# Performance work log

Hardware: AMD Instinct MI355X
Metric: run time of the kernel (lower is better)

Reference implementation:

```python
import jax, jax.numpy as jnp
import numpy as np
import math

B, N, WIDTH, HEADS = 2, 2048, 1024, 16
ATTN_CH = WIDTH // HEADS  # 64 (note: width//heads//3 of the 3*width fused dim)


def setup_inputs() -> dict:
    key = jax.random.key(0)
    ks = jax.random.split(key, 3)
    std = 0.02
    return {
        "x": jax.random.normal(ks[0], (B, N, WIDTH), dtype=jnp.float32),
        "w_qkv": jax.random.normal(ks[1], (WIDTH, 3 * WIDTH), dtype=jnp.float32) * std,
        "b_qkv": jnp.zeros((3 * WIDTH,), dtype=jnp.float32),
        "w_proj": jax.random.normal(ks[2], (WIDTH, WIDTH), dtype=jnp.float32) * std,
        "b_proj": jnp.zeros((WIDTH,), dtype=jnp.float32),
    }


def reference(x, w_qkv, b_qkv, w_proj, b_proj):
    bs, n_ctx, width = x.shape
    qkv = x @ w_qkv + b_qkv                       # [b, n, 3*width]
    attn_ch = (3 * width) // HEADS // 3           # head dim
    scale = 1.0 / math.sqrt(math.sqrt(attn_ch))
    # per-head layout: [b, n, heads, 3*attn_ch] -> split q,k,v
    qkv = qkv.reshape(bs, n_ctx, HEADS, 3 * attn_ch)
    q, k, v = jnp.split(qkv, 3, axis=-1)          # each [b, n, h, c]
    weight = jnp.einsum("bthc,bshc->bhts", q * scale, k * scale)
    weight = jax.nn.softmax(weight.astype(jnp.float32), axis=-1).astype(qkv.dtype)
    out = jnp.einsum("bhts,bshc->bthc", weight, v).reshape(bs, n_ctx, -1)
    return out @ w_proj + b_proj
```

## Files before the change

### kernel.cpp

```cpp
#include <hip/hip_runtime.h>
#include <hip/hip_fp16.h>

#define BATCH 2
#define NCTX  2048
#define WIDTH 1024
#define HEADS 16
#define CH    64
#define QKVD  (3 * WIDTH)
#define MROWS (BATCH * NCTX)

typedef __attribute__((ext_vector_type(4))) float    f32x4;
typedef __attribute__((ext_vector_type(8))) _Float16 f16x8;

#define QSCALE 0.18033688011112042f

__device__ __forceinline__ void gll16(void* lds, const void* g) {
    __builtin_amdgcn_global_load_lds(
        (const __attribute__((address_space(1))) unsigned int*)g,
        (__attribute__((address_space(3))) unsigned int*)lds, 16, 0, 0);
}

__device__ __forceinline__ unsigned pkrtz(float a, float b) {
    auto p = __builtin_amdgcn_cvt_pkrtz(a, b);
    return __builtin_bit_cast(unsigned, p);
}

__global__ __launch_bounds__(256)
void split_x_f16(const float* __restrict__ x, __half* __restrict__ tiles)
{
    const int mb = blockIdx.x, kt = blockIdx.y;
    const int t = threadIdx.x;
    __half* tb = (__half*)tiles + ((size_t)mb * 32 + kt) * 4096;
    #pragma unroll
    for (int it = 0; it < 2; ++it) {
        const int idx = it * 256 + t;
        const int m = idx >> 2, q = idx & 3;
        const float* src = x + (size_t)(mb * 128 + m) * WIDTH + kt * 32 + q * 8;
        const f32x4 v0 = *(const f32x4*)src;
        const f32x4 v1 = *(const f32x4*)(src + 4);
        f16x8 h;
        #pragma unroll
        for (int j = 0; j < 4; ++j) { h[j] = (_Float16)v0[j]; h[4 + j] = (_Float16)v1[j]; }
        *(f16x8*)&tb[(q * 128 + m) * 8] = h;
    }
}

__global__ __launch_bounds__(256)
void split_w_f16(const float* __restrict__ w, __half* __restrict__ tiles, int N)
{
    __shared__ float tile[32][129];
    const int nb = blockIdx.x, kt = blockIdx.y;
    const int t = threadIdx.x;
    #pragma unroll
    for (int it = 0; it < 2; ++it) {
        const int idx = it * 256 + t;
        const int kk = idx >> 4, n8 = idx & 15;
        const float* src = w + (size_t)(kt * 32 + kk) * N + nb * 128 + n8 * 8;
        #pragma unroll
        for (int j = 0; j < 8; ++j) tile[kk][n8 * 8 + j] = src[j];
    }
    __syncthreads();
    __half* tb = tiles + ((size_t)nb * 32 + kt) * 4096;
    #pragma unroll
    for (int it = 0; it < 2; ++it) {
        const int idx = it * 256 + t;
        const int q = idx >> 7, nn = idx & 127;
        f16x8 h;
        #pragma unroll
        for (int j = 0; j < 8; ++j) h[j] = (_Float16)tile[q * 8 + j][nn];
        *(f16x8*)&tb[(q * 128 + nn) * 8] = h;
    }
}

__global__ __launch_bounds__(256)
void gemm_qkv(const __half* __restrict__ At, const __half* __restrict__ Bt,
              const float* __restrict__ bias,
              __half* __restrict__ qg, __half* __restrict__ kg, __half* __restrict__ vtg)
{
    __shared__ __align__(16) _Float16 sm[16384];
    const int t = threadIdx.x, lane = t & 63, w = t >> 6;
    const int lq = lane & 15, quad = lane >> 4;
    const int nb = blockIdx.x, mb = blockIdx.y;
    const int wm = (w >> 1) * 64, wn = (w & 1) * 64;

    const __half* Ab = At + ((size_t)mb * 32) * 4096;
    const __half* Bb = Bt + ((size_t)nb * 32) * 4096;
    const int c0 = w * 4;

    f32x4 acc[4][4];
    #pragma unroll
    for (int i = 0; i < 4; ++i)
        #pragma unroll
        for (int j = 0; j < 4; ++j) acc[i][j] = 0;

    f16x8 pf[4];
    #pragma unroll
    for (int i = 0; i < 4; ++i) {
        const int c = c0 + i;
        const __half* g = (c < 8 ? Ab + c * 512 : Bb + (c - 8) * 512) + lane * 8;
        pf[i] = *(const f16x8*)g;
    }
    #pragma unroll
    for (int i = 0; i < 4; ++i)
        *(f16x8*)&sm[(c0 + i) * 512 + lane * 8] = pf[i];
    __syncthreads();

    for (int kt = 0; kt < 32; ++kt) {
        _Float16* cur = sm + (kt & 1) * 8192;
        _Float16* nxt = sm + ((kt + 1) & 1) * 8192;

        if (kt + 1 < 32) {
            #pragma unroll
            for (int i = 0; i < 4; ++i) {
                const int c = c0 + i;
                const __half* g = (c < 8 ? Ab + (size_t)(kt + 1) * 4096 + c * 512
                                         : Bb + (size_t)(kt + 1) * 4096 + (c - 8) * 512) + lane * 8;
                pf[i] = *(const f16x8*)g;
            }
        }

        f16x8 a[4], b[4];
        #pragma unroll
        for (int i = 0; i < 4; ++i) {
            a[i] = *(const f16x8*)&cur[(quad * 128 + wm + i * 16 + lq) * 8];
            b[i] = *(const f16x8*)&cur[4096 + (quad * 128 + wn + i * 16 + lq) * 8];
        }
        #pragma unroll
        for (int i = 0; i < 4; ++i)
            #pragma unroll
            for (int j = 0; j < 4; ++j)
                acc[i][j] = __builtin_amdgcn_mfma_f32_16x16x32_f16(a[i], b[j], acc[i][j], 0, 0, 0);

        if (kt + 1 < 32) {
            #pragma unroll
            for (int i = 0; i < 4; ++i)
                *(f16x8*)&nxt[(c0 + i) * 512 + lane * 8] = pf[i];
        }
        __syncthreads();
    }

    const int bb = mb >> 4;
    #pragma unroll
    for (int jf = 0; jf < 4; ++jf) {
        const int col = nb * 128 + wn + jf * 16 + lq;
        const int h = col / 192;
        const int sect = col - h * 192;
        const int type = sect >> 6;
        const int c = sect & 63;
        const float bv = bias[col];
        const size_t bh = (size_t)bb * 16 + h;
        #pragma unroll
        for (int i = 0; i < 4; ++i) {
            #pragma unroll
            for (int r = 0; r < 4; ++r) {
                const int n = (mb & 15) * 128 + wm + i * 16 + quad * 4 + r;
                const float v = acc[i][jf][r] + bv;
                if (type == 0) {
                    const size_t a2 = ((bh * 16 + (n >> 7)) * 8 + (c >> 3)) * 1024
                                      + (size_t)(n & 127) * 8 + (c & 7);
                    qg[a2] = __float2half(v * QSCALE);
                } else if (type == 1) {
                    const size_t a2 = ((bh * 32 + (n >> 6)) * 8 + (c >> 3)) * 512
                                      + (size_t)(n & 63) * 8 + (c & 7);
                    kg[a2] = __float2half(v);
                } else {
                    const size_t a2 = ((bh * 32 + (n >> 6)) * 8 + ((n >> 3) & 7)) * 512
                                      + (size_t)c * 8 + (n & 7);
                    vtg[a2] = __float2half(v);
                }
            }
        }
    }
}

__global__ __launch_bounds__(256)
void attn_mfma5(const __half* __restrict__ qg, const __half* __restrict__ kg,
                const __half* __restrict__ vtg, __half* __restrict__ a2)
{
    __shared__ __align__(16) _Float16 Ks[2][4096];
    __shared__ __align__(16) _Float16 Vt[2][4096];
    __shared__ __align__(16) _Float16 Ps[4096];

    const int t = threadIdx.x, lane = t & 63, w = t >> 6;
    const int lq = lane & 15, quad = lane >> 4;
    const int bid = blockIdx.x;
    const int qt = (bid >> 3) & 31;
    const int bh_ = (bid & 7) + ((bid >> 8) << 3);
    const size_t bh = (size_t)bh_;
    const int h = bh_ & 15, b = bh_ >> 4;

    const __half* qtile = qg + (bh * 16 + (qt >> 1)) * 8192 + (size_t)(qt & 1) * 512;
    const __half* kbase = kg + bh * 32 * 4096;
    const __half* vbase = vtg + bh * 32 * 4096;

    #pragma unroll
    for (int i = 0; i < 2; ++i)
        gll16((void*)&Ps[(w * 2 + i) * 512],
              (const void*)(qtile + (size_t)(w * 2 + i) * 1024 + lane * 8));

    const int lw = w * 1024 + lane * 8;
    f16x8 kpf[2], vpf[2];
    #pragma unroll
    for (int i = 0; i < 2; ++i) {
        kpf[i] = *(const f16x8*)(kbase + lw + i * 512);
        vpf[i] = *(const f16x8*)(vbase + lw + i * 512);
    }
    __syncthreads();

    #pragma unroll
    for (int i = 0; i < 2; ++i) {
        *(f16x8*)&Ks[0][lw + i * 512] = kpf[i];
        *(f16x8*)&Vt[0][lw + i * 512] = vpf[i];
    }
    f16x8 aq[2];
    #pragma unroll
    for (int ks = 0; ks < 2; ++ks)
        aq[ks] = *(const f16x8*)&Ps[((ks * 4 + quad) * 64 + w * 16 + lq) * 8];
    __syncthreads();

    f32x4 O[4], Ol;
    Ol = 0;
    #pragma unroll
    for (int j = 0; j < 4; ++j) O[j] = 0;
    f16x8 ones;
    #pragma unroll
    for (int j = 0; j < 8; ++j) ones[j] = (_Float16)1.0f;

    _Float16* Pw = &Ps[w * 1024];
    const int kb_hi = quad >> 1, joff = (quad & 1) * 4;
    const f32x4 zc = {0.0f, 0.0f, 0.0f, 0.0f};

    const __half* kp = kbase + 4096 + lw;
    const __half* vp = vbase + 4096 + lw;

    for (int kt = 0; kt < 32; ++kt) {
        const int cur = kt & 1;

        if (kt < 31) {
            kpf[0] = *(const f16x8*)(kp);
            kpf[1] = *(const f16x8*)(kp + 512);
            vpf[0] = *(const f16x8*)(vp);
            vpf[1] = *(const f16x8*)(vp + 512);
            kp += 4096; vp += 4096;
        }

        f32x4 st[4];
        #pragma unroll
        for (int mt = 0; mt < 4; ++mt) {
            f16x8 kf0 = *(const f16x8*)&Ks[cur][((quad) * 64 + mt * 16 + lq) * 8];
            f16x8 kf1 = *(const f16x8*)&Ks[cur][((4 + quad) * 64 + mt * 16 + lq) * 8];
            st[mt] = __builtin_amdgcn_mfma_f32_16x16x32_f16(kf0, aq[0], zc, 0, 0, 0);
            st[mt] = __builtin_amdgcn_mfma_f32_16x16x32_f16(kf1, aq[1], st[mt], 0, 0, 0);
        }

        #pragma unroll
        for (int mt = 0; mt < 4; ++mt) {
            const float e0 = __builtin_amdgcn_exp2f(st[mt][0]);
            const float e1 = __builtin_amdgcn_exp2f(st[mt][1]);
            const float e2 = __builtin_amdgcn_exp2f(st[mt][2]);
            const float e3 = __builtin_amdgcn_exp2f(st[mt][3]);
            uint2 pk;
            pk.x = pkrtz(e0, e1);
            pk.y = pkrtz(e2, e3);
            *(uint2*)&Pw[((mt * 2 + kb_hi) * 16 + lq) * 8 + joff] = pk;
        }

        #pragma unroll
        for (int ks = 0; ks < 2; ++ks) {
            f16x8 ap = *(const f16x8*)&Pw[((ks * 4 + quad) * 16 + lq) * 8];
            Ol = __builtin_amdgcn_mfma_f32_16x16x32_f16(ap, ones, Ol, 0, 0, 0);
            #pragma unroll
            for (int jc = 0; jc < 4; ++jc) {
                f16x8 vf = *(const f16x8*)&Vt[cur][((ks * 4 + quad) * 64 + jc * 16 + lq) * 8];
                O[jc] = __builtin_amdgcn_mfma_f32_16x16x32_f16(ap, vf, O[jc], 0, 0, 0);
            }
        }

        if (kt < 31) {
            *(f16x8*)&Ks[cur ^ 1][lw]       = kpf[0];
            *(f16x8*)&Ks[cur ^ 1][lw + 512] = kpf[1];
            *(f16x8*)&Vt[cur ^ 1][lw]       = vpf[0];
            *(f16x8*)&Vt[cur ^ 1][lw + 512] = vpf[1];
        }
        __syncthreads();
    }

    float linv[4];
    #pragma unroll
    for (int r = 0; r < 4; ++r) linv[r] = 1.0f / Ol[r];

    __half* a2t = a2 + ((size_t)(b * 16 + (qt >> 1)) * 32) * 4096;
    const int mbase = (qt & 1) * 64 + w * 16 + quad * 4;
    #pragma unroll
    for (int jc = 0; jc < 4; ++jc) {
        const int ch = h * 64 + jc * 16 + lq;
        const int ktp = ch >> 5;
        const int qc = (ch >> 3) & 3;
        const int j = ch & 7;
        #pragma unroll
        for (int r = 0; r < 4; ++r) {
            a2t[(size_t)ktp * 4096 + (qc * 128 + mbase + r) * 8 + j] =
                __float2half(O[jc][r] * linv[r]);
        }
    }
}

__global__ __launch_bounds__(256)
void gemm_proj(const __half* __restrict__ At, const __half* __restrict__ Bt,
               const float* __restrict__ bias, float* __restrict__ out)
{
    __shared__ __align__(16) _Float16 sm[16384];
    const int t = threadIdx.x, lane = t & 63, w = t >> 6;
    const int lq = lane & 15, quad = lane >> 4;
    const int nb = blockIdx.x, mb = blockIdx.y;
    const int wm = (w >> 1) * 64, wn = (w & 1) * 64;

    const __half* Ab = At + ((size_t)mb * 32) * 4096;
    const __half* Bb = Bt + ((size_t)nb * 32) * 4096;
    const int c0 = w * 4;

    f32x4 acc[4][4];
    #pragma unroll
    for (int i = 0; i < 4; ++i)
        #pragma unroll
        for (int j = 0; j < 4; ++j) acc[i][j] = 0;

    f16x8 pf[4];
    #pragma unroll
    for (int i = 0; i < 4; ++i) {
        const int c = c0 + i;
        const __half* g = (c < 8 ? Ab + c * 512 : Bb + (c - 8) * 512) + lane * 8;
        pf[i] = *(const f16x8*)g;
    }
    #pragma unroll
    for (int i = 0; i < 4; ++i)
        *(f16x8*)&sm[(c0 + i) * 512 + lane * 8] = pf[i];
    __syncthreads();

    for (int kt = 0; kt < 32; ++kt) {
        _Float16* cur = sm + (kt & 1) * 8192;
        _Float16* nxt = sm + ((kt + 1) & 1) * 8192;

        if (kt + 1 < 32) {
            #pragma unroll
            for (int i = 0; i < 4; ++i) {
                const int c = c0 + i;
                const __half* g = (c < 8 ? Ab + (size_t)(kt + 1) * 4096 + c * 512
                                         : Bb + (size_t)(kt + 1) * 4096 + (c - 8) * 512) + lane * 8;
                pf[i] = *(const f16x8*)g;
            }
        }

        f16x8 a[4], b[4];
        #pragma unroll
        for (int i = 0; i < 4; ++i) {
            a[i] = *(const f16x8*)&cur[(quad * 128 + wm + i * 16 + lq) * 8];
            b[i] = *(const f16x8*)&cur[4096 + (quad * 128 + wn + i * 16 + lq) * 8];
        }
        #pragma unroll
        for (int i = 0; i < 4; ++i)
            #pragma unroll
            for (int j = 0; j < 4; ++j)
                acc[i][j] = __builtin_amdgcn_mfma_f32_16x16x32_f16(a[i], b[j], acc[i][j], 0, 0, 0);

        if (kt + 1 < 32) {
            #pragma unroll
            for (int i = 0; i < 4; ++i)
                *(f16x8*)&nxt[(c0 + i) * 512 + lane * 8] = pf[i];
        }
        __syncthreads();
    }

    #pragma unroll
    for (int jf = 0; jf < 4; ++jf) {
        const int col = nb * 128 + wn + jf * 16 + lq;
        const float bv = bias[col];
        #pragma unroll
        for (int i = 0; i < 4; ++i)
            #pragma unroll
            for (int r = 0; r < 4; ++r) {
                const int row = mb * 128 + wm + i * 16 + quad * 4 + r;
                out[(size_t)row * WIDTH + col] = acc[i][jf][r] + bv;
            }
    }
}

extern "C" void kernel_launch(void* const* d_in, const int* in_sizes, int n_in,
                              void* d_out, int out_size, void* d_ws, size_t ws_size,
                              hipStream_t stream)
{
    const float* x      = (const float*)d_in[0];
    const float* w_qkv  = (const float*)d_in[1];
    const float* b_qkv  = (const float*)d_in[2];
    const float* w_proj = (const float*)d_in[3];
    const float* b_proj = (const float*)d_in[4];
    float* out = (float*)d_out;

    char* p = (char*)d_ws;
    size_t o = 0;
    __half* A1  = (__half*)(p + o); o += (size_t)MROWS * WIDTH * 2;
    __half* Bq  = (__half*)(p + o); o += (size_t)WIDTH * QKVD * 2;
    __half* Qg  = (__half*)(p + o); o += (size_t)MROWS * WIDTH * 2;
    __half* Kg  = (__half*)(p + o); o += (size_t)MROWS * WIDTH * 2;
    __half* Vtg = (__half*)(p + o); o += (size_t)MROWS * WIDTH * 2;
    __half* A2  = (__half*)(p + o); o += (size_t)MROWS * WIDTH * 2;
    __half* Bp  = (__half*)(p + o); o += (size_t)WIDTH * WIDTH * 2;

    dim3 blk(256);

    split_x_f16<<<dim3(32, 32), blk, 0, stream>>>(x, A1);
    split_w_f16<<<dim3(24, 32), blk, 0, stream>>>(w_qkv, Bq, QKVD);
    split_w_f16<<<dim3(8, 32),  blk, 0, stream>>>(w_proj, Bp, WIDTH);

    gemm_qkv<<<dim3(24, 32), blk, 0, stream>>>(A1, Bq, b_qkv, Qg, Kg, Vtg);

    attn_mfma5<<<dim3(1024), blk, 0, stream>>>(Qg, Kg, Vtg, A2);

    gemm_proj<<<dim3(8, 32), blk, 0, stream>>>(A2, Bp, b_proj, out);
}
```

Baseline: 205.5 us.

## Split attention KV range across waves with register-direct loads and LDS reduction

The attention kernel now gives each wave all 64 query rows of the block and a quarter of each key tile, instead of 16 query rows and the full tile. K and V fragments are loaded straight from global into registers, and the P fragment is fed to the 16x16x16 MFMA from registers, so the double-buffered LDS staging of K/V/P and the per-tile barriers go away. Partial row sums and output accumulators are then reduced across waves through LDS in two passes. This avoids the unnormalised max-free softmax rescale, but raises register pressure (64 accumulator regs plus Q fragments), uses uncoalesced 8-byte V loads, and adds an end-of-kernel reduction.

```diff
diff --git a/kernel.cpp b/kernel.cpp
--- a/kernel.cpp
+++ b/kernel.cpp
@@ -11,14 +11,9 @@
 
 typedef __attribute__((ext_vector_type(4))) float    f32x4;
 typedef __attribute__((ext_vector_type(8))) _Float16 f16x8;
+typedef __attribute__((ext_vector_type(4))) _Float16 f16x4;
 
 #define QSCALE 0.18033688011112042f
-
-__device__ __forceinline__ void gll16(void* lds, const void* g) {
-    __builtin_amdgcn_global_load_lds(
-        (const __attribute__((address_space(1))) unsigned int*)g,
-        (__attribute__((address_space(3))) unsigned int*)lds, 16, 0, 0);
-}
 
 __device__ __forceinline__ unsigned pkrtz(float a, float b) {
     auto p = __builtin_amdgcn_cvt_pkrtz(a, b);
@@ -174,12 +169,11 @@
 }
 
 __global__ __launch_bounds__(256)
-void attn_mfma5(const __half* __restrict__ qg, const __half* __restrict__ kg,
+void attn_mfma7(const __half* __restrict__ qg, const __half* __restrict__ kg,
                 const __half* __restrict__ vtg, __half* __restrict__ a2)
 {
-    __shared__ __align__(16) _Float16 Ks[2][4096];
-    __shared__ __align__(16) _Float16 Vt[2][4096];
-    __shared__ __align__(16) _Float16 Ps[4096];
+    __shared__ __align__(16) float red[4][3][2][16][16];
+    __shared__ __align__(16) float rol[4][3][16];
 
     const int t = threadIdx.x, lane = t & 63, w = t >> 6;
     const int lq = lane & 15, quad = lane >> 4;
@@ -189,119 +183,139 @@
     const size_t bh = (size_t)bh_;
     const int h = bh_ & 15, b = bh_ >> 4;
 
-    const __half* qtile = qg + (bh * 16 + (qt >> 1)) * 8192 + (size_t)(qt & 1) * 512;
+    const __half* qtile = qg + (bh * 16 + (qt >> 1)) * 8192;
     const __half* kbase = kg + bh * 32 * 4096;
     const __half* vbase = vtg + bh * 32 * 4096;
 
-    #pragma unroll
-    for (int i = 0; i < 2; ++i)
-        gll16((void*)&Ps[(w * 2 + i) * 512],
-              (const void*)(qtile + (size_t)(w * 2 + i) * 1024 + lane * 8));
-
-    const int lw = w * 1024 + lane * 8;
-    f16x8 kpf[2], vpf[2];
-    #pragma unroll
-    for (int i = 0; i < 2; ++i) {
-        kpf[i] = *(const f16x8*)(kbase + lw + i * 512);
-        vpf[i] = *(const f16x8*)(vbase + lw + i * 512);
-    }
-    __syncthreads();
-
-    #pragma unroll
-    for (int i = 0; i < 2; ++i) {
-        *(f16x8*)&Ks[0][lw + i * 512] = kpf[i];
-        *(f16x8*)&Vt[0][lw + i * 512] = vpf[i];
-    }
-    f16x8 aq[2];
-    #pragma unroll
-    for (int ks = 0; ks < 2; ++ks)
-        aq[ks] = *(const f16x8*)&Ps[((ks * 4 + quad) * 64 + w * 16 + lq) * 8];
-    __syncthreads();
-
-    f32x4 O[4], Ol;
-    Ol = 0;
-    #pragma unroll
-    for (int j = 0; j < 4; ++j) O[j] = 0;
-    f16x8 ones;
-    #pragma unroll
-    for (int j = 0; j < 8; ++j) ones[j] = (_Float16)1.0f;
-
-    _Float16* Pw = &Ps[w * 1024];
-    const int kb_hi = quad >> 1, joff = (quad & 1) * 4;
+    const int qrow0 = (qt & 1) * 64;
+    f16x8 aq[4][2];
+    #pragma unroll
+    for (int qn = 0; qn < 4; ++qn)
+        #pragma unroll
+        for (int ks = 0; ks < 2; ++ks)
+            aq[qn][ks] = *(const f16x8*)(qtile + (size_t)(ks * 4 + quad) * 1024
+                                         + (qrow0 + qn * 16 + lq) * 8);
+
+    const int kofs0 = ((0 * 4 + quad) * 64 + w * 16 + lq) * 8;
+    const int kofs1 = ((1 * 4 + quad) * 64 + w * 16 + lq) * 8;
+    int vofs[4];
+    #pragma unroll
+    for (int jc = 0; jc < 4; ++jc)
+        vofs[jc] = ((w * 2 + (quad >> 1)) * 64 + jc * 16 + lq) * 8 + (quad & 1) * 4;
+
+    f32x4 O[4][4], Ol[4];
+    #pragma unroll
+    for (int qn = 0; qn < 4; ++qn) {
+        Ol[qn] = 0;
+        #pragma unroll
+        for (int jc = 0; jc < 4; ++jc) O[qn][jc] = 0;
+    }
+    f16x4 ones4;
+    #pragma unroll
+    for (int j = 0; j < 4; ++j) ones4[j] = (_Float16)1.0f;
     const f32x4 zc = {0.0f, 0.0f, 0.0f, 0.0f};
 
-    const __half* kp = kbase + 4096 + lw;
-    const __half* vp = vbase + 4096 + lw;
+    f16x8 kf0 = *(const f16x8*)(kbase + kofs0);
+    f16x8 kf1 = *(const f16x8*)(kbase + kofs1);
+    f16x4 vf[4];
+    #pragma unroll
+    for (int jc = 0; jc < 4; ++jc) vf[jc] = *(const f16x4*)(vbase + vofs[jc]);
+
+    const __half* kp = kbase + 4096;
+    const __half* vp = vbase + 4096;
 
     for (int kt = 0; kt < 32; ++kt) {
-        const int cur = kt & 1;
-
+        f16x8 kn0, kn1; f16x4 vn[4];
         if (kt < 31) {
-            kpf[0] = *(const f16x8*)(kp);
-            kpf[1] = *(const f16x8*)(kp + 512);
-            vpf[0] = *(const f16x8*)(vp);
-            vpf[1] = *(const f16x8*)(vp + 512);
+            kn0 = *(const f16x8*)(kp + kofs0);
+            kn1 = *(const f16x8*)(kp + kofs1);
+            #pragma unroll
+            for (int jc = 0; jc < 4; ++jc) vn[jc] = *(const f16x4*)(vp + vofs[jc]);
             kp += 4096; vp += 4096;
         }
 
-        f32x4 st[4];
-        #pragma unroll
-        for (int mt = 0; mt < 4; ++mt) {
-            f16x8 kf0 = *(const f16x8*)&Ks[cur][((quad) * 64 + mt * 16 + lq) * 8];
-            f16x8 kf1 = *(const f16x8*)&Ks[cur][((4 + quad) * 64 + mt * 16 + lq) * 8];
-            st[mt] = __builtin_amdgcn_mfma_f32_16x16x32_f16(kf0, aq[0], zc, 0, 0, 0);
-            st[mt] = __builtin_amdgcn_mfma_f32_16x16x32_f16(kf1, aq[1], st[mt], 0, 0, 0);
-        }
-
-        #pragma unroll
-        for (int mt = 0; mt < 4; ++mt) {
-            const float e0 = __builtin_amdgcn_exp2f(st[mt][0]);
-            const float e1 = __builtin_amdgcn_exp2f(st[mt][1]);
-            const float e2 = __builtin_amdgcn_exp2f(st[mt][2]);
-            const float e3 = __builtin_amdgcn_exp2f(st[mt][3]);
+        #pragma unroll
+        for (int qn = 0; qn < 4; ++qn) {
+            f32x4 st = __builtin_amdgcn_mfma_f32_16x16x32_f16(kf0, aq[qn][0], zc, 0, 0, 0);
+            st = __builtin_amdgcn_mfma_f32_16x16x32_f16(kf1, aq[qn][1], st, 0, 0, 0);
+            const float e0 = __builtin_amdgcn_exp2f(st[0]);
+            const float e1 = __builtin_amdgcn_exp2f(st[1]);
+            const float e2 = __builtin_amdgcn_exp2f(st[2]);
+            const float e3 = __builtin_amdgcn_exp2f(st[3]);
             uint2 pk;
             pk.x = pkrtz(e0, e1);
             pk.y = pkrtz(e2, e3);
-            *(uint2*)&Pw[((mt * 2 + kb_hi) * 16 + lq) * 8 + joff] = pk;
-        }
-
-        #pragma unroll
-        for (int ks = 0; ks < 2; ++ks) {
-            f16x8 ap = *(const f16x8*)&Pw[((ks * 4 + quad) * 16 + lq) * 8];
-            Ol = __builtin_amdgcn_mfma_f32_16x16x32_f16(ap, ones, Ol, 0, 0, 0);
-            #pragma unroll
-            for (int jc = 0; jc < 4; ++jc) {
-                f16x8 vf = *(const f16x8*)&Vt[cur][((ks * 4 + quad) * 64 + jc * 16 + lq) * 8];
-                O[jc] = __builtin_amdgcn_mfma_f32_16x16x32_f16(ap, vf, O[jc], 0, 0, 0);
-            }
+            const f16x4 pa = __builtin_bit_cast(f16x4, pk);
+            Ol[qn] = __builtin_amdgcn_mfma_f32_16x16x16f16(pa, ones4, Ol[qn], 0, 0, 0);
+            #pragma unroll
+            for (int jc = 0; jc < 4; ++jc)
+                O[qn][jc] = __builtin_amdgcn_mfma_f32_16x16x16f16(pa, vf[jc], O[qn][jc], 0, 0, 0);
         }
 
         if (kt < 31) {
-            *(f16x8*)&Ks[cur ^ 1][lw]       = kpf[0];
-            *(f16x8*)&Ks[cur ^ 1][lw + 512] = kpf[1];
-            *(f16x8*)&Vt[cur ^ 1][lw]       = vpf[0];
-            *(f16x8*)&Vt[cur ^ 1][lw + 512] = vpf[1];
-        }
-        __syncthreads();
-    }
-
+            kf0 = kn0; kf1 = kn1;
+            #pragma unroll
+            for (int jc = 0; jc < 4; ++jc) vf[jc] = vn[jc];
+        }
+    }
+
+    #pragma unroll
+    for (int qn = 0; qn < 4; ++qn) {
+        if (qn == w) continue;
+        const int rel = (w < qn) ? w : w - 1;
+        if (lq == 0)
+            *(f32x4*)&rol[qn][rel][quad * 4] = Ol[qn];
+        *(f32x4*)&red[qn][rel][0][lq][quad * 4] = O[qn][0];
+        *(f32x4*)&red[qn][rel][1][lq][quad * 4] = O[qn][1];
+    }
+    __syncthreads();
+
+    f32x4 lt = Ol[w];
+    #pragma unroll
+    for (int s = 0; s < 3; ++s) lt += *(const f32x4*)&rol[w][s][quad * 4];
     float linv[4];
     #pragma unroll
-    for (int r = 0; r < 4; ++r) linv[r] = 1.0f / Ol[r];
+    for (int r = 0; r < 4; ++r) linv[r] = 1.0f / lt[r];
 
     __half* a2t = a2 + ((size_t)(b * 16 + (qt >> 1)) * 32) * 4096;
-    const int mbase = (qt & 1) * 64 + w * 16 + quad * 4;
-    #pragma unroll
-    for (int jc = 0; jc < 4; ++jc) {
-        const int ch = h * 64 + jc * 16 + lq;
-        const int ktp = ch >> 5;
-        const int qc = (ch >> 3) & 3;
-        const int j = ch & 7;
-        #pragma unroll
-        for (int r = 0; r < 4; ++r) {
-            a2t[(size_t)ktp * 4096 + (qc * 128 + mbase + r) * 8 + j] =
-                __float2half(O[jc][r] * linv[r]);
-        }
+    const int mb0 = (qt & 1) * 64 + w * 16 + quad * 4;
+
+    #pragma unroll
+    for (int jj = 0; jj < 2; ++jj) {
+        f32x4 s = O[w][jj];
+        #pragma unroll
+        for (int src = 0; src < 3; ++src)
+            s += *(const f32x4*)&red[w][src][jj][lq][quad * 4];
+        const int ch = h * 64 + jj * 16 + lq;
+        const int ktp = ch >> 5, qc = (ch >> 3) & 3, j = ch & 7;
+        #pragma unroll
+        for (int r = 0; r < 4; ++r)
+            a2t[(size_t)ktp * 4096 + (qc * 128 + mb0 + r) * 8 + j] =
+                __float2half(s[r] * linv[r]);
+    }
+    __syncthreads();
+
+    #pragma unroll
+    for (int qn = 0; qn < 4; ++qn) {
+        if (qn == w) continue;
+        const int rel = (w < qn) ? w : w - 1;
+        *(f32x4*)&red[qn][rel][0][lq][quad * 4] = O[qn][2];
+        *(f32x4*)&red[qn][rel][1][lq][quad * 4] = O[qn][3];
+    }
+    __syncthreads();
+
+    #pragma unroll
+    for (int jj = 0; jj < 2; ++jj) {
+        f32x4 s = O[w][2 + jj];
+        #pragma unroll
+        for (int src = 0; src < 3; ++src)
+            s += *(const f32x4*)&red[w][src][jj][lq][quad * 4];
+        const int ch = h * 64 + (2 + jj) * 16 + lq;
+        const int ktp = ch >> 5, qc = (ch >> 3) & 3, j = ch & 7;
+        #pragma unroll
+        for (int r = 0; r < 4; ++r)
+            a2t[(size_t)ktp * 4096 + (qc * 128 + mb0 + r) * 8 + j] =
+                __float2half(s[r] * linv[r]);
     }
 }
 
@@ -414,7 +428,7 @@
 
     gemm_qkv<<<dim3(24, 32), blk, 0, stream>>>(A1, Bq, b_qkv, Qg, Kg, Vtg);
 
-    attn_mfma5<<<dim3(1024), blk, 0, stream>>>(Qg, Kg, Vtg, A2);
+    attn_mfma7<<<dim3(1024), blk, 0, stream>>>(Qg, Kg, Vtg, A2);
 
     gemm_proj<<<dim3(8, 32), blk, 0, stream>>>(A2, Bp, b_proj, out);
 }
```

Measured after the change: 217.5 us. 5.8% more time.
